# Kernel optimization log

Measured on AMD Instinct MI355X. Metric: run time of the kernel, lower is better.

Reference implementation:

```python
import jax, jax.numpy as jnp
import numpy as np

EPS = 1e-12


def setup_inputs() -> dict:
    key = jax.random.key(0)
    N, C, H, W = 32, 256, 56, 56
    k1, k2, k3 = jax.random.split(key, 3)
    x = jax.random.normal(k1, (N, C, H, W), dtype=jnp.float32)
    weight = 1.0 + 0.1 * jax.random.normal(k2, (C,), dtype=jnp.float32)
    bias = 0.1 * jax.random.normal(k3, (C,), dtype=jnp.float32)
    # Variable group sizes summing to C=256 (16 groups)
    gs = np.array([8, 24, 8, 16, 32, 16, 8, 8, 16, 24, 8, 16, 16, 8, 32, 16], dtype=np.int64)
    assert gs.sum() == C
    # Per-sample channel permutation expressed as row indices into x.view(N*C, H*W)
    rng = np.random.default_rng(0)
    perms = np.stack([rng.permutation(C) for _ in range(N)])  # [N, C]
    offs = np.arange(N)[:, None] * C
    indexes = (perms + offs).reshape(-1).astype(np.int64)
    inv = np.argsort(perms, axis=1)
    reverse_indexes = (inv + offs).reshape(-1).astype(np.int64)
    return {
        "x": x,
        "weight": weight,
        "bias": bias,
        "group_sizes": jnp.asarray(gs),
        "indexes": jnp.asarray(indexes),
        "reverse_indexes": jnp.asarray(reverse_indexes),
    }


def reference(x, weight, bias, group_sizes, indexes, reverse_indexes):
    N, C, H, W = x.shape
    HW = H * W
    gs = np.asarray(group_sizes)          # static group layout
    G = gs.shape[0]
    seg = jnp.asarray(np.repeat(np.arange(G), gs))  # [C] channel -> group id
    n = jnp.asarray(gs * HW, dtype=x.dtype)         # [G] elements per group

    # gather: per-sample channel permutation
    xg = x.reshape(N * C, HW)[indexes].reshape(N, C, HW)

    # per-group mean via segmented reduction over channels
    s1 = xg.sum(axis=2)                                    # [N, C]
    mu_g = jax.ops.segment_sum(s1.T, seg, num_segments=G).T / n      # [N, G]
    mu_c = mu_g[:, seg]                                    # [N, C]

    diff = xg - mu_c[:, :, None]
    s2 = (diff * diff).sum(axis=2)                         # [N, C]
    # torch.var default is unbiased -> divide by (n - 1)
    var_g = jax.ops.segment_sum(s2.T, seg, num_segments=G).T / (n - 1.0)
    ivar_c = (1.0 / jnp.sqrt(var_g + EPS))[:, seg]         # [N, C]

    out = diff * ivar_c[:, :, None] * weight[None, :, None] + bias[None, :, None]

    # scatter back to original channel order
    out = out.reshape(N * C, HW)[reverse_indexes].reshape(N, C, H, W)
    return out
```

## Files before the change

kernel.cpp:

```cpp
#include <hip/hip_runtime.h>

#define N_ 32
#define C_ 256
#define G_ 16
#define HW_ 3136
#define HW4_ 784
#define EPS_ 1e-12f

typedef float vf4 __attribute__((ext_vector_type(4)));
typedef float vf2 __attribute__((ext_vector_type(2)));

__device__ __forceinline__ int rd_int(const int* __restrict__ p, int i, bool is64) {
    return is64 ? p[2 * i] : p[i];
}

__device__ __forceinline__ void acc4(const vf4 v, float& s, float& s2) {
    s += v.x + v.y + v.z + v.w;
    s2 = fmaf(v.x, v.x, s2);
    s2 = fmaf(v.y, v.y, s2);
    s2 = fmaf(v.z, v.z, s2);
    s2 = fmaf(v.w, v.w, s2);
}

__device__ __forceinline__ vf4 aff(const vf4 v, float sc, float sh) {
    vf4 r;
    r.x = fmaf(v.x, sc, sh);
    r.y = fmaf(v.y, sc, sh);
    r.z = fmaf(v.z, sc, sh);
    r.w = fmaf(v.w, sc, sh);
    return r;
}


__global__ __launch_bounds__(256, 8) void vgn_reduce(
    const float* __restrict__ x,
    const int*   __restrict__ indexes,
    const int*   __restrict__ group_sizes,
    float*       __restrict__ rsums)
{
    const bool is64 = (group_sizes[1] == 0);
    const int t  = threadIdx.x;
    const int r0 = blockIdx.x * 2;

    const int src0 = rd_int(indexes, r0,     is64);
    const int src1 = rd_int(indexes, r0 + 1, is64);
    const vf4* p0 = (const vf4*)x + (size_t)src0 * HW4_;
    const vf4* p1 = (const vf4*)x + (size_t)src1 * HW4_;

    vf4 a0 = p0[t], b0 = p0[t + 256], c0 = p0[t + 512];
    vf4 a1 = p1[t], b1 = p1[t + 256], c1 = p1[t + 512];

    float sA = 0.f, qA = 0.f, sB = 0.f, qB = 0.f;
    if (t < 16) {
        vf4 d0 = p0[768 + t];
        vf4 d1 = p1[768 + t];
        acc4(d0, sA, qA);
        acc4(d1, sB, qB);
    }
    acc4(a0, sA, qA); acc4(b0, sA, qA); acc4(c0, sA, qA);
    acc4(a1, sB, qB); acc4(b1, sB, qB); acc4(c1, sB, qB);

    #pragma unroll
    for (int off = 32; off > 0; off >>= 1) {
        sA += __shfl_down(sA, off);
        qA += __shfl_down(qA, off);
        sB += __shfl_down(sB, off);
        qB += __shfl_down(qB, off);
    }

    __shared__ float red[4][4];
    if ((t & 63) == 0) {
        const int w = t >> 6;
        red[w][0] = sA; red[w][1] = qA; red[w][2] = sB; red[w][3] = qB;
    }
    __syncthreads();
    if (t < 4)
        rsums[r0 * 2 + t] = red[0][t] + red[1][t] + red[2][t] + red[3][t];
}

__global__ __launch_bounds__(256, 8) void vgn_norm(
    const float* __restrict__ x,
    const int*   __restrict__ indexes,
    const int*   __restrict__ group_sizes,
    const float* __restrict__ weight,
    const float* __restrict__ bias,
    const float* __restrict__ rsums,
    float*       __restrict__ out)
{
    const bool is64 = (group_sizes[1] == 0);
    const int t  = threadIdx.x;
    const int r0 = blockIdx.x * 2;
    const int n  = r0 >> 8;

    const int src0 = rd_int(indexes, r0,     is64);
    const int src1 = rd_int(indexes, r0 + 1, is64);
    const vf4* p0 = (const vf4*)x + (size_t)src0 * HW4_;
    const vf4* p1 = (const vf4*)x + (size_t)src1 * HW4_;
    vf4* o0 = (vf4*)out + (size_t)src0 * HW4_;
    vf4* o1 = (vf4*)out + (size_t)src1 * HW4_;

    vf4 a0 = p0[t], b0 = p0[t + 256], c0 = p0[t + 512];
    vf4 a1 = p1[t], b1 = p1[t + 256], c1 = p1[t + 512];
    vf4 d0, d1;
    const bool tail = (t < 16);
    if (tail) { d0 = p0[768 + t]; d1 = p1[768 + t]; }

    __shared__ float sScale[2], sShift[2];
    if (t < 64) {
        const int half = t >> 5;
        const int l    = t & 31;
        const int j    = (r0 + half) & 255;
        int g = 0, P = 0, Pg = 0;
        #pragma unroll
        for (int k = 0; k < G_; k++) {
            P += rd_int(group_sizes, k, is64);
            if (j >= P) { g++; Pg = P; }
        }
        const int gsz = rd_int(group_sizes, g, is64);
        float a = 0.f, b = 0.f;
        if (l < gsz) {
            const vf2 pr = ((const vf2*)rsums)[n * C_ + Pg + l];
            a = pr.x; b = pr.y;
        }
        #pragma unroll
        for (int off = 16; off > 0; off >>= 1) {
            a += __shfl_down(a, off, 32);
            b += __shfl_down(b, off, 32);
        }
        if (l == 0) {
            const float cnt = (float)gsz * (float)HW_;
            const float mu  = a / cnt;
            const float var = (b - mu * a) / (cnt - 1.0f);
            const float ivr = rsqrtf(var + EPS_);
            const float sc  = ivr * weight[j];
            sScale[half] = sc;
            sShift[half] = fmaf(-mu, sc, bias[j]);
        }
    }
    __syncthreads();

    const float sc0 = sScale[0], sh0 = sShift[0];
    const float sc1 = sScale[1], sh1 = sShift[1];

    __builtin_nontemporal_store(aff(a0, sc0, sh0), o0 + t);
    __builtin_nontemporal_store(aff(b0, sc0, sh0), o0 + t + 256);
    __builtin_nontemporal_store(aff(c0, sc0, sh0), o0 + t + 512);
    __builtin_nontemporal_store(aff(a1, sc1, sh1), o1 + t);
    __builtin_nontemporal_store(aff(b1, sc1, sh1), o1 + t + 256);
    __builtin_nontemporal_store(aff(c1, sc1, sh1), o1 + t + 512);
    if (tail) {
        __builtin_nontemporal_store(aff(d0, sc0, sh0), o0 + 768 + t);
        __builtin_nontemporal_store(aff(d1, sc1, sh1), o1 + 768 + t);
    }
}

extern "C" void kernel_launch(void* const* d_in, const int* in_sizes, int n_in,
                              void* d_out, int out_size, void* d_ws, size_t ws_size,
                              hipStream_t stream) {
    const float* x           = (const float*)d_in[0];
    const float* weight      = (const float*)d_in[1];
    const float* bias        = (const float*)d_in[2];
    const int*   group_sizes = (const int*)  d_in[3];
    const int*   indexes     = (const int*)  d_in[4];

    float* rsums = (float*)d_ws;

    dim3 grid(N_ * C_ / 2), block(256);
    vgn_reduce<<<grid, block, 0, stream>>>(x, indexes, group_sizes, rsums);
    vgn_norm  <<<grid, block, 0, stream>>>(x, indexes, group_sizes,
                                           weight, bias, rsums, (float*)d_out);
}
```

Measured before the change: 202.3 us.

## Fuse reduce and normalize into one cooperative kernel with grid sync

```diff
diff --git a/kernel.cpp b/kernel.cpp
--- a/kernel.cpp
+++ b/kernel.cpp
@@ -1,4 +1,7 @@
 #include <hip/hip_runtime.h>
+#include <hip/hip_cooperative_groups.h>
+
+namespace cg = cooperative_groups;
 
 #define N_ 32
 #define C_ 256
@@ -6,6 +9,8 @@
 #define HW_ 3136
 #define HW4_ 784
 #define EPS_ 1e-12f
+#define RPB_ 4
+#define GRID_ (N_ * C_ / RPB_)
 
 typedef float vf4 __attribute__((ext_vector_type(4)));
 typedef float vf2 __attribute__((ext_vector_type(2)));
@@ -32,126 +37,135 @@
 }
 
 
-__global__ __launch_bounds__(256, 8) void vgn_reduce(
-    const float* __restrict__ x,
-    const int*   __restrict__ indexes,
-    const int*   __restrict__ group_sizes,
-    float*       __restrict__ rsums)
+__device__ __forceinline__ void row_reduce(
+    const float* __restrict__ x, const int* __restrict__ indexes,
+    bool is64, int row, int lane, float* __restrict__ rsums)
+{
+    const int src = rd_int(indexes, row, is64);
+    const vf4* p = (const vf4*)x + (size_t)src * HW4_;
+
+    float s = 0.f, q = 0.f;
+    #pragma unroll
+    for (int h = 0; h < 2; h++) {
+        vf4 v0 = p[lane + (h * 6 + 0) * 64];
+        vf4 v1 = p[lane + (h * 6 + 1) * 64];
+        vf4 v2 = p[lane + (h * 6 + 2) * 64];
+        vf4 v3 = p[lane + (h * 6 + 3) * 64];
+        vf4 v4 = p[lane + (h * 6 + 4) * 64];
+        vf4 v5 = p[lane + (h * 6 + 5) * 64];
+        acc4(v0, s, q); acc4(v1, s, q); acc4(v2, s, q);
+        acc4(v3, s, q); acc4(v4, s, q); acc4(v5, s, q);
+    }
+    if (lane < 16) {
+        vf4 t = p[768 + lane];
+        acc4(t, s, q);
+    }
+    #pragma unroll
+    for (int off = 32; off > 0; off >>= 1) {
+        s += __shfl_down(s, off);
+        q += __shfl_down(q, off);
+    }
+    if (lane == 0) {
+        vf2 r; r.x = s; r.y = q;
+        ((vf2*)rsums)[row] = r;
+    }
+}
+
+__device__ __forceinline__ void row_norm(
+    const float* __restrict__ x, const int* __restrict__ indexes,
+    const int* __restrict__ group_sizes,
+    const float* __restrict__ weight, const float* __restrict__ bias,
+    const float* __restrict__ rsums, float* __restrict__ out,
+    bool is64, int row, int lane)
+{
+    const int j = row & (C_ - 1);
+    const int n = row >> 8;
+
+    int g = 0, P = 0, Pg = 0;
+    #pragma unroll
+    for (int k = 0; k < G_; k++) {
+        P += rd_int(group_sizes, k, is64);
+        if (j >= P) { g++; Pg = P; }
+    }
+    const int gsz = rd_int(group_sizes, g, is64);
+
+    float a = 0.f, b = 0.f;
+    if (lane < gsz) {
+        const vf2 pr = ((const vf2*)rsums)[n * C_ + Pg + lane];
+        a = pr.x; b = pr.y;
+    }
+    #pragma unroll
+    for (int off = 32; off > 0; off >>= 1) {
+        a += __shfl_down(a, off);
+        b += __shfl_down(b, off);
+    }
+    a = __shfl(a, 0);
+    b = __shfl(b, 0);
+
+    const float cnt = (float)gsz * (float)HW_;
+    const float mu  = a / cnt;
+    const float var = (b - mu * a) / (cnt - 1.0f);
+    const float sc  = rsqrtf(var + EPS_) * weight[j];
+    const float sh  = fmaf(-mu, sc, bias[j]);
+
+    const int src = rd_int(indexes, row, is64);
+    const vf4* p = (const vf4*)x + (size_t)src * HW4_;
+    vf4*       o = (vf4*)out      + (size_t)src * HW4_;
+
+    #pragma unroll
+    for (int h = 0; h < 2; h++) {
+        vf4 v0 = p[lane + (h * 6 + 0) * 64];
+        vf4 v1 = p[lane + (h * 6 + 1) * 64];
+        vf4 v2 = p[lane + (h * 6 + 2) * 64];
+        vf4 v3 = p[lane + (h * 6 + 3) * 64];
+        vf4 v4 = p[lane + (h * 6 + 4) * 64];
+        vf4 v5 = p[lane + (h * 6 + 5) * 64];
+        o[lane + (h * 6 + 0) * 64] = aff(v0, sc, sh);
+        o[lane + (h * 6 + 1) * 64] = aff(v1, sc, sh);
+        o[lane + (h * 6 + 2) * 64] = aff(v2, sc, sh);
+        o[lane + (h * 6 + 3) * 64] = aff(v3, sc, sh);
+        o[lane + (h * 6 + 4) * 64] = aff(v4, sc, sh);
+        o[lane + (h * 6 + 5) * 64] = aff(v5, sc, sh);
+    }
+    if (lane < 16)
+        o[768 + lane] = aff(p[768 + lane], sc, sh);
+}
+
+__global__ __launch_bounds__(256, 8) void vgn_coop(
+    const float* __restrict__ x, const int* __restrict__ indexes,
+    const int* __restrict__ group_sizes,
+    const float* __restrict__ weight, const float* __restrict__ bias,
+    float* __restrict__ rsums, float* __restrict__ out)
 {
     const bool is64 = (group_sizes[1] == 0);
-    const int t  = threadIdx.x;
-    const int r0 = blockIdx.x * 2;
+    const int wave = threadIdx.x >> 6;
+    const int lane = threadIdx.x & 63;
+    const int row  = blockIdx.x * RPB_ + wave;
 
-    const int src0 = rd_int(indexes, r0,     is64);
-    const int src1 = rd_int(indexes, r0 + 1, is64);
-    const vf4* p0 = (const vf4*)x + (size_t)src0 * HW4_;
-    const vf4* p1 = (const vf4*)x + (size_t)src1 * HW4_;
-
-    vf4 a0 = p0[t], b0 = p0[t + 256], c0 = p0[t + 512];
-    vf4 a1 = p1[t], b1 = p1[t + 256], c1 = p1[t + 512];
-
-    float sA = 0.f, qA = 0.f, sB = 0.f, qB = 0.f;
-    if (t < 16) {
-        vf4 d0 = p0[768 + t];
-        vf4 d1 = p1[768 + t];
-        acc4(d0, sA, qA);
-        acc4(d1, sB, qB);
-    }
-    acc4(a0, sA, qA); acc4(b0, sA, qA); acc4(c0, sA, qA);
-    acc4(a1, sB, qB); acc4(b1, sB, qB); acc4(c1, sB, qB);
-
-    #pragma unroll
-    for (int off = 32; off > 0; off >>= 1) {
-        sA += __shfl_down(sA, off);
-        qA += __shfl_down(qA, off);
-        sB += __shfl_down(sB, off);
-        qB += __shfl_down(qB, off);
-    }
-
-    __shared__ float red[4][4];
-    if ((t & 63) == 0) {
-        const int w = t >> 6;
-        red[w][0] = sA; red[w][1] = qA; red[w][2] = sB; red[w][3] = qB;
-    }
-    __syncthreads();
-    if (t < 4)
-        rsums[r0 * 2 + t] = red[0][t] + red[1][t] + red[2][t] + red[3][t];
+    row_reduce(x, indexes, is64, row, lane, rsums);
+    cg::this_grid().sync();
+    row_norm(x, indexes, group_sizes, weight, bias, rsums, out, is64, row, lane);
 }
 
-__global__ __launch_bounds__(256, 8) void vgn_norm(
-    const float* __restrict__ x,
-    const int*   __restrict__ indexes,
-    const int*   __restrict__ group_sizes,
-    const float* __restrict__ weight,
-    const float* __restrict__ bias,
-    const float* __restrict__ rsums,
-    float*       __restrict__ out)
+__global__ __launch_bounds__(256, 8) void vgn_p1(
+    const float* __restrict__ x, const int* __restrict__ indexes,
+    const int* __restrict__ group_sizes, float* __restrict__ rsums)
 {
     const bool is64 = (group_sizes[1] == 0);
-    const int t  = threadIdx.x;
-    const int r0 = blockIdx.x * 2;
-    const int n  = r0 >> 8;
+    const int row = blockIdx.x * RPB_ + (threadIdx.x >> 6);
+    row_reduce(x, indexes, is64, row, threadIdx.x & 63, rsums);
+}
 
-    const int src0 = rd_int(indexes, r0,     is64);
-    const int src1 = rd_int(indexes, r0 + 1, is64);
-    const vf4* p0 = (const vf4*)x + (size_t)src0 * HW4_;
-    const vf4* p1 = (const vf4*)x + (size_t)src1 * HW4_;
-    vf4* o0 = (vf4*)out + (size_t)src0 * HW4_;
-    vf4* o1 = (vf4*)out + (size_t)src1 * HW4_;
-
-    vf4 a0 = p0[t], b0 = p0[t + 256], c0 = p0[t + 512];
-    vf4 a1 = p1[t], b1 = p1[t + 256], c1 = p1[t + 512];
-    vf4 d0, d1;
-    const bool tail = (t < 16);
-    if (tail) { d0 = p0[768 + t]; d1 = p1[768 + t]; }
-
-    __shared__ float sScale[2], sShift[2];
-    if (t < 64) {
-        const int half = t >> 5;
-        const int l    = t & 31;
-        const int j    = (r0 + half) & 255;
-        int g = 0, P = 0, Pg = 0;
-        #pragma unroll
-        for (int k = 0; k < G_; k++) {
-            P += rd_int(group_sizes, k, is64);
-            if (j >= P) { g++; Pg = P; }
-        }
-        const int gsz = rd_int(group_sizes, g, is64);
-        float a = 0.f, b = 0.f;
-        if (l < gsz) {
-            const vf2 pr = ((const vf2*)rsums)[n * C_ + Pg + l];
-            a = pr.x; b = pr.y;
-        }
-        #pragma unroll
-        for (int off = 16; off > 0; off >>= 1) {
-            a += __shfl_down(a, off, 32);
-            b += __shfl_down(b, off, 32);
-        }
-        if (l == 0) {
-            const float cnt = (float)gsz * (float)HW_;
-            const float mu  = a / cnt;
-            const float var = (b - mu * a) / (cnt - 1.0f);
-            const float ivr = rsqrtf(var + EPS_);
-            const float sc  = ivr * weight[j];
-            sScale[half] = sc;
-            sShift[half] = fmaf(-mu, sc, bias[j]);
-        }
-    }
-    __syncthreads();
-
-    const float sc0 = sScale[0], sh0 = sShift[0];
-    const float sc1 = sScale[1], sh1 = sShift[1];
-
-    __builtin_nontemporal_store(aff(a0, sc0, sh0), o0 + t);
-    __builtin_nontemporal_store(aff(b0, sc0, sh0), o0 + t + 256);
-    __builtin_nontemporal_store(aff(c0, sc0, sh0), o0 + t + 512);
-    __builtin_nontemporal_store(aff(a1, sc1, sh1), o1 + t);
-    __builtin_nontemporal_store(aff(b1, sc1, sh1), o1 + t + 256);
-    __builtin_nontemporal_store(aff(c1, sc1, sh1), o1 + t + 512);
-    if (tail) {
-        __builtin_nontemporal_store(aff(d0, sc0, sh0), o0 + 768 + t);
-        __builtin_nontemporal_store(aff(d1, sc1, sh1), o1 + 768 + t);
-    }
+__global__ __launch_bounds__(256, 8) void vgn_p2(
+    const float* __restrict__ x, const int* __restrict__ indexes,
+    const int* __restrict__ group_sizes,
+    const float* __restrict__ weight, const float* __restrict__ bias,
+    const float* __restrict__ rsums, float* __restrict__ out)
+{
+    const bool is64 = (group_sizes[1] == 0);
+    const int row = blockIdx.x * RPB_ + (threadIdx.x >> 6);
+    row_norm(x, indexes, group_sizes, weight, bias, rsums, out, is64,
+             row, threadIdx.x & 63);
 }
 
 extern "C" void kernel_launch(void* const* d_in, const int* in_sizes, int n_in,
@@ -164,9 +178,18 @@
     const int*   indexes     = (const int*)  d_in[4];
 
     float* rsums = (float*)d_ws;
+    float* outp  = (float*)d_out;
 
-    dim3 grid(N_ * C_ / 2), block(256);
-    vgn_reduce<<<grid, block, 0, stream>>>(x, indexes, group_sizes, rsums);
-    vgn_norm  <<<grid, block, 0, stream>>>(x, indexes, group_sizes,
-                                           weight, bias, rsums, (float*)d_out);
+    void* args[] = { (void*)&x, (void*)&indexes, (void*)&group_sizes,
+                     (void*)&weight, (void*)&bias, (void*)&rsums, (void*)&outp };
+
+    hipError_t err = hipLaunchCooperativeKernel(
+        (const void*)vgn_coop, dim3(GRID_), dim3(256), args, 0, stream);
+
+    if (err != hipSuccess) {
+        vgn_p1<<<dim3(GRID_), dim3(256), 0, stream>>>(x, indexes, group_sizes,
+                                                      rsums);
+        vgn_p2<<<dim3(GRID_), dim3(256), 0, stream>>>(x, indexes, group_sizes,
+                                                      weight, bias, rsums, outp);
+    }
 }
```

Measured after the change: 429.0 us. 2.12x slower.
